# Kernel optimization log

Hardware: AMD Instinct MI355X
Metric: run time of the kernel (lower is better)

The kernel has to match this reference:

```python
import jax, jax.numpy as jnp
import numpy as np

B, T, D = 4096, 200, 128
K_SHORT = 5


def setup_inputs() -> dict:
    key = jax.random.key(0)
    ks = jax.random.split(key, 8)
    hist_items = jax.random.normal(ks[0], (B, T, D), dtype=jnp.float32)
    hist_mask = jax.random.randint(ks[1], (B, T), 0, 2).astype(bool)
    hist_mask = hist_mask.at[:, 0].set(True)  # avoid fully-masked rows
    hist_age_hours = jax.random.uniform(ks[2], (B, T), dtype=jnp.float32) * 168.0
    hist_popularity = jax.random.uniform(ks[3], (B, T), dtype=jnp.float32)
    s = 1.0 / float(np.sqrt(D))
    Wq = jax.random.normal(ks[4], (D, D), dtype=jnp.float32) * s
    Wk = jax.random.normal(ks[5], (D, D), dtype=jnp.float32) * s
    Wv = jax.random.normal(ks[6], (D, D), dtype=jnp.float32) * s
    gate_w = jax.random.normal(ks[7], (1, 2), dtype=jnp.float32) * 0.5
    gate_b = jnp.zeros((1,), dtype=jnp.float32)
    ln_gamma = jnp.ones((D,), dtype=jnp.float32)
    ln_beta = jnp.zeros((D,), dtype=jnp.float32)
    decay_alpha = jnp.asarray(0.05, dtype=jnp.float32)
    return {"hist_items": hist_items, "hist_mask": hist_mask,
            "hist_age_hours": hist_age_hours, "hist_popularity": hist_popularity,
            "Wq": Wq, "Wk": Wk, "Wv": Wv, "gate_w": gate_w, "gate_b": gate_b,
            "ln_gamma": ln_gamma, "ln_beta": ln_beta, "decay_alpha": decay_alpha}


def reference(hist_items, hist_mask, hist_age_hours, hist_popularity,
              Wq, Wk, Wv, gate_w, gate_b, ln_gamma, ln_beta, decay_alpha):
    dt = hist_items.dtype
    maskf = hist_mask.astype(dt)  # (B,T)
    # learnable time-decay bias
    alpha = jax.nn.softplus(decay_alpha) + 1e-6
    decay = jnp.exp(-alpha * hist_age_hours) * maskf  # (B,T)
    # masked mean of history as the single query
    mean_hist = (hist_items * maskf[..., None]).sum(1) / (maskf.sum(1, keepdims=True) + 1e-6)  # (B,D)
    q = mean_hist @ Wq.T                                # (B,D)
    k = jnp.einsum('btd,ed->bte', hist_items, Wk)       # (B,T,D)
    v = jnp.einsum('btd,ed->bte', hist_items, Wv)       # (B,T,D)
    scale = 1.0 / float(np.sqrt(hist_items.shape[-1]))
    scores = jnp.einsum('bd,btd->bt', q, k) * scale + jnp.log(decay + 1e-12)
    scores = jnp.where(hist_mask, scores, -jnp.inf)
    attn = jax.nn.softmax(scores, axis=-1)              # (B,T)
    long_term = jnp.einsum('bt,btd->bd', attn, v)       # (B,D)
    # vectorized last-K window: positions [cnt-K, cnt)
    cnt = jnp.maximum(hist_mask.sum(1), 1)              # (B,) int
    K = min(K_SHORT, hist_items.shape[1])
    ar = jnp.arange(hist_items.shape[1])[None, :]       # (1,T)
    lastk = (ar >= (cnt[:, None] - K)) & (ar < cnt[:, None])  # (B,T) bool
    lk = lastk.astype(dt)
    denom = jnp.maximum(lk.sum(1, keepdims=True), 1.0)  # (B,1)
    short_term = (hist_items * lk[..., None]).sum(1) / denom  # (B,D)
    mean_pop = (hist_popularity * lk).sum(1) / denom[:, 0]
    mean_rec = (hist_age_hours * lk).sum(1) / denom[:, 0]
    ctx = jnp.stack([mean_pop, mean_rec], axis=-1)      # (B,2)
    g = jax.nn.sigmoid(ctx @ gate_w.T + gate_b)         # (B,1)
    user = g * short_term + (1.0 - g) * long_term       # (B,D)
    # LayerNorm (eps=1e-5, biased variance, matching torch)
    mu = user.mean(-1, keepdims=True)
    var = user.var(-1, keepdims=True)
    return (user - mu) / jnp.sqrt(var + 1e-5) * ln_gamma + ln_beta
```

## Files before the change

kernel.cpp:

```cpp
#include <hip/hip_runtime.h>

#define BB 4096
#define TT 200
#define DD 128
#define KSHORT 5
#define RTRIPS 13

__global__ void precompute_A_kernel(const float* __restrict__ Wq,
                                    const float* __restrict__ Wk,
                                    float* __restrict__ A,
                                    const unsigned* __restrict__ m,
                                    int* __restrict__ flag) {
  __shared__ int s_bad;
  const int d = blockIdx.x, dp = threadIdx.x;
  float acc = 0.f;
#pragma unroll 8
  for (int e = 0; e < DD; ++e) acc += Wk[e * DD + d] * Wq[e * DD + dp];
  A[d * DD + dp] = acc * 0.08838834764831845f;
  if (blockIdx.x == 0) {
    if (dp == 0) s_bad = 0;
    __syncthreads();
    unsigned bad = 0;
#pragma unroll
    for (int i = dp; i < 1024; i += DD) bad |= (m[i] > 1u) ? 1u : 0u;
    if (bad) atomicOr(&s_bad, 1);
    __syncthreads();
    if (dp == 0) *flag = s_bad;
  }
}

__global__ __launch_bounds__(256, 4) void fused_kernel(
    const float* __restrict__ items, const void* __restrict__ maskp,
    const float* __restrict__ age, const float* __restrict__ pop,
    const float* __restrict__ Wv, const float* __restrict__ gate_w,
    const float* __restrict__ gate_b, const float* __restrict__ gamma,
    const float* __restrict__ beta, const float* __restrict__ alpha_in,
    const float* __restrict__ A, const int* __restrict__ flagp,
    float* __restrict__ out) {
  __shared__ int   s_idx[TT];
  __shared__ float s_wm[TT], s_ww[TT], s_df[TT];
  __shared__ float s_pa[8 * DD];
  __shared__ float s_pb[8 * DD];
  __shared__ float s_mean[DD], s_qk[DD], s_w[DD], s_user[DD];
  __shared__ float s_l[8];
  __shared__ float s_scal[6];
  __shared__ int   s_wt[4];

  const int b = blockIdx.x, tid = threadIdx.x;
  const int lane32 = tid & 31, stream = tid >> 5;
  const int mode = *flagp;

  float mymask = 0.f, myage = 0.f;
  if (tid < TT) {
    int mk = mode ? (int)((const unsigned char*)maskp)[(size_t)b * TT + tid]
                  : ((const int*)maskp)[(size_t)b * TT + tid];
    mymask = mk ? 1.f : 0.f;
    myage = age[(size_t)b * TT + tid];
    s_wm[tid] = mymask;
  } else if (tid == TT) {
    s_scal[2] = log1pf(expf(alpha_in[0])) + 1e-6f;
  }
  __syncthreads();

  if (tid < 64) {
    float c = 0.f;
    for (int t = tid; t < TT; t += 64) c += s_wm[t];
#pragma unroll
    for (int o = 32; o > 0; o >>= 1) c += __shfl_xor(c, o);
    if (tid == 0) s_scal[0] = c;
  }
  __syncthreads();

  const float cntf = s_scal[0];
  const int cnt = max((int)(cntf + 0.5f), 1);
  const int lo = max(cnt - KSHORT, 0);
  const float dn = (float)(cnt - lo);

  const bool inw = (tid < TT) && (tid >= lo) && (tid < cnt);
  const bool need = (tid < TT) && (mymask > 0.f || inw);
  const unsigned long long bal = __ballot(need);
  const int lane64 = tid & 63, wv = tid >> 6;
  const int within = __popcll(bal & ((1ULL << lane64) - 1ULL));
  if (lane64 == 0) s_wt[wv] = __popcll(bal);
  __syncthreads();

  int off = 0;
#pragma unroll
  for (int w2 = 0; w2 < 3; ++w2) off += (w2 < wv) ? s_wt[w2] : 0;
  const int n = s_wt[0] + s_wt[1] + s_wt[2] + s_wt[3];
  if (need) {
    const int p = off + within;
    const float al = s_scal[2];
    s_idx[p] = tid;
    s_wm[p] = mymask;
    s_ww[p] = inw ? 1.f : 0.f;
    s_df[p] = (mymask > 0.f) ? (__expf(-al * myage) + 1e-12f) : 0.f;
  }
  __syncthreads();

  const float* rowbase = items + (size_t)b * (TT * DD) + lane32 * 4;
  float4 r[RTRIPS];
  float4 ms = {0.f, 0.f, 0.f, 0.f}, ss = {0.f, 0.f, 0.f, 0.f};
#pragma unroll
  for (int j = 0; j < RTRIPS; ++j) {
    const int i = stream + j * 8;
    float4 v = {0.f, 0.f, 0.f, 0.f};
    float wm = 0.f, ww = 0.f;
    if (i < n) {
      const int t = s_idx[i];
      wm = s_wm[i];
      ww = s_ww[i];
      v = *(const float4*)(rowbase + t * DD);
    }
    r[j] = v;
    ms.x += wm * v.x; ms.y += wm * v.y; ms.z += wm * v.z; ms.w += wm * v.w;
    ss.x += ww * v.x; ss.y += ww * v.y; ss.z += ww * v.z; ss.w += ww * v.w;
  }
  for (int i = stream + RTRIPS * 8; i < n; i += 8) {
    const int t = s_idx[i];
    const float wm = s_wm[i], ww = s_ww[i];
    const float4 v = *(const float4*)(rowbase + t * DD);
    ms.x += wm * v.x; ms.y += wm * v.y; ms.z += wm * v.z; ms.w += wm * v.w;
    ss.x += ww * v.x; ss.y += ww * v.y; ss.z += ww * v.z; ss.w += ww * v.w;
  }
  *(float4*)&s_pa[stream * DD + lane32 * 4] = ms;
  *(float4*)&s_pb[stream * DD + lane32 * 4] = ss;
  __syncthreads();

  float short_v = 0.f;
  if (tid < DD) {
    float am = 0.f, as = 0.f;
#pragma unroll
    for (int s = 0; s < 8; ++s) { am += s_pa[s * DD + tid]; as += s_pb[s * DD + tid]; }
    s_mean[tid] = am / (cntf + 1e-6f);
    short_v = as / dn;
  } else if (tid == DD) {
    float sp = 0.f, sr = 0.f;
    for (int t = lo; t < cnt; ++t) {
      sp += pop[(size_t)b * TT + t];
      sr += age[(size_t)b * TT + t];
    }
    const float z = gate_w[0] * (sp / dn) + gate_w[1] * (sr / dn) + gate_b[0];
    s_scal[1] = 1.f / (1.f + expf(-z));
  }
  __syncthreads();

  if (tid < DD) {
    const float4* Ar = (const float4*)(A + tid * DD);
    float acc = 0.f;
#pragma unroll
    for (int j = 0; j < DD / 4; ++j) {
      const float4 a4 = Ar[j];
      acc += a4.x * s_mean[4 * j] + a4.y * s_mean[4 * j + 1] +
             a4.z * s_mean[4 * j + 2] + a4.w * s_mean[4 * j + 3];
    }
    s_qk[tid] = acc;
  }
  __syncthreads();

  const float4 qk = *(const float4*)&s_qk[lane32 * 4];
  float l = 0.f;
  float4 o = {0.f, 0.f, 0.f, 0.f};
#pragma unroll
  for (int j = 0; j < RTRIPS; ++j) {
    const int i = stream + j * 8;
    if (i < n) {
      const float df = s_df[i];
      const float4 v = r[j];
      float p = qk.x * v.x + qk.y * v.y + qk.z * v.z + qk.w * v.w;
      p += __shfl_xor(p, 1);
      p += __shfl_xor(p, 2);
      p += __shfl_xor(p, 4);
      p += __shfl_xor(p, 8);
      p += __shfl_xor(p, 16);
      const float e = __expf(p) * df;
      l += e;
      o.x += e * v.x; o.y += e * v.y; o.z += e * v.z; o.w += e * v.w;
    }
  }
  for (int i = stream + RTRIPS * 8; i < n; i += 8) {
    const int t = s_idx[i];
    const float df = s_df[i];
    const float4 v = *(const float4*)(rowbase + t * DD);
    float p = qk.x * v.x + qk.y * v.y + qk.z * v.z + qk.w * v.w;
    p += __shfl_xor(p, 1);
    p += __shfl_xor(p, 2);
    p += __shfl_xor(p, 4);
    p += __shfl_xor(p, 8);
    p += __shfl_xor(p, 16);
    const float e = __expf(p) * df;
    l += e;
    o.x += e * v.x; o.y += e * v.y; o.z += e * v.z; o.w += e * v.w;
  }
  *(float4*)&s_pa[stream * DD + lane32 * 4] = o;
  if (lane32 == 0) s_l[stream] = l;
  __syncthreads();

  if (tid < DD) {
    float O = 0.f;
#pragma unroll
    for (int s = 0; s < 8; ++s) O += s_pa[s * DD + tid];
    float L = 0.f;
#pragma unroll
    for (int s = 0; s < 8; ++s) L += s_l[s];
    s_w[tid] = O / L;
  }
  __syncthreads();

  if (tid < DD) {
    const float4* Wr = (const float4*)(Wv + tid * DD);
    float acc = 0.f;
#pragma unroll
    for (int j = 0; j < DD / 4; ++j) {
      const float4 a4 = Wr[j];
      acc += a4.x * s_w[4 * j] + a4.y * s_w[4 * j + 1] +
             a4.z * s_w[4 * j + 2] + a4.w * s_w[4 * j + 3];
    }
    const float g = s_scal[1];
    s_user[tid] = g * short_v + (1.f - g) * acc;
  }
  __syncthreads();

  if (tid < 64) {
    const float x0 = s_user[tid], x1 = s_user[64 + tid];
    float su = x0 + x1;
#pragma unroll
    for (int off2 = 32; off2 > 0; off2 >>= 1) su += __shfl_xor(su, off2);
    const float mu = su * (1.f / 128.f);
    const float d0 = x0 - mu, d1 = x1 - mu;
    float s2 = d0 * d0 + d1 * d1;
#pragma unroll
    for (int off2 = 32; off2 > 0; off2 >>= 1) s2 += __shfl_xor(s2, off2);
    if (tid == 0) {
      s_scal[4] = mu;
      s_scal[5] = 1.f / sqrtf(s2 * (1.f / 128.f) + 1e-5f);
    }
  }
  __syncthreads();

  if (tid < DD) {
    out[(size_t)b * DD + tid] =
        (s_user[tid] - s_scal[4]) * s_scal[5] * gamma[tid] + beta[tid];
  }
}

extern "C" void kernel_launch(void* const* d_in, const int* in_sizes, int n_in,
                              void* d_out, int out_size, void* d_ws, size_t ws_size,
                              hipStream_t stream) {
  const float* items  = (const float*)d_in[0];
  const void*  maskp  = d_in[1];
  const float* age    = (const float*)d_in[2];
  const float* pop    = (const float*)d_in[3];
  const float* Wq     = (const float*)d_in[4];
  const float* Wk     = (const float*)d_in[5];
  const float* Wv     = (const float*)d_in[6];
  const float* gate_w = (const float*)d_in[7];
  const float* gate_b = (const float*)d_in[8];
  const float* gamma  = (const float*)d_in[9];
  const float* beta   = (const float*)d_in[10];
  const float* alpha  = (const float*)d_in[11];

  char* ws = (char*)d_ws;
  int*   flag = (int*)ws;
  float* A    = (float*)(ws + 256);
  float* outp = (float*)d_out;

  precompute_A_kernel<<<DD, DD, 0, stream>>>(Wq, Wk, A, (const unsigned*)maskp, flag);
  fused_kernel<<<BB, 256, 0, stream>>>(items, maskp, age, pop, Wv, gate_w,
                                       gate_b, gamma, beta, alpha, A, flag,
                                       outp);
}
```

Before: 589.1 us.

## Fold precompute kernel into fused kernel with per-block q and Wk^T q

Removes the separate precompute launch that formed A = Wk^T Wq and the mask-format flag. Each block now checks the mask format itself, computes q = Wq·mean and then u = Wk^T q in two matvec stages, and counts the mask with a ballot popcount instead of a shared-memory reduction. It also caches the window's popularity and age values in shared memory for the gate. The aim is to save a kernel launch and the dependency between the two kernels. The cost is two matvecs per block instead of one, plus extra barriers, across 4096 blocks.

Result: slower. 603.9 us (+2.5%).

```diff
diff --git a/kernel.cpp b/kernel.cpp
--- a/kernel.cpp
+++ b/kernel.cpp
@@ -6,49 +6,39 @@
 #define KSHORT 5
 #define RTRIPS 13
 
-__global__ void precompute_A_kernel(const float* __restrict__ Wq,
-                                    const float* __restrict__ Wk,
-                                    float* __restrict__ A,
-                                    const unsigned* __restrict__ m,
-                                    int* __restrict__ flag) {
-  __shared__ int s_bad;
-  const int d = blockIdx.x, dp = threadIdx.x;
-  float acc = 0.f;
-#pragma unroll 8
-  for (int e = 0; e < DD; ++e) acc += Wk[e * DD + d] * Wq[e * DD + dp];
-  A[d * DD + dp] = acc * 0.08838834764831845f;
-  if (blockIdx.x == 0) {
-    if (dp == 0) s_bad = 0;
-    __syncthreads();
-    unsigned bad = 0;
-#pragma unroll
-    for (int i = dp; i < 1024; i += DD) bad |= (m[i] > 1u) ? 1u : 0u;
-    if (bad) atomicOr(&s_bad, 1);
-    __syncthreads();
-    if (dp == 0) *flag = s_bad;
-  }
-}
-
 __global__ __launch_bounds__(256, 4) void fused_kernel(
     const float* __restrict__ items, const void* __restrict__ maskp,
     const float* __restrict__ age, const float* __restrict__ pop,
+    const float* __restrict__ Wq, const float* __restrict__ Wk,
     const float* __restrict__ Wv, const float* __restrict__ gate_w,
     const float* __restrict__ gate_b, const float* __restrict__ gamma,
     const float* __restrict__ beta, const float* __restrict__ alpha_in,
-    const float* __restrict__ A, const int* __restrict__ flagp,
     float* __restrict__ out) {
   __shared__ int   s_idx[TT];
-  __shared__ float s_wm[TT], s_ww[TT], s_df[TT];
+  __shared__ float s_cwm[TT], s_cww[TT], s_cdf[TT];
   __shared__ float s_pa[8 * DD];
   __shared__ float s_pb[8 * DD];
-  __shared__ float s_mean[DD], s_qk[DD], s_w[DD], s_user[DD];
+  __shared__ float s_mean[DD], s_q[DD], s_u[DD], s_w[DD], s_user[DD];
+  __shared__ float s_pop[KSHORT], s_agw[KSHORT];
   __shared__ float s_l[8];
   __shared__ float s_scal[6];
-  __shared__ int   s_wt[4];
+  __shared__ int   s_cm[4], s_wt[4];
+  __shared__ int   s_mode;
 
   const int b = blockIdx.x, tid = threadIdx.x;
   const int lane32 = tid & 31, stream = tid >> 5;
-  const int mode = *flagp;
+  const int lane64 = tid & 63, wv = tid >> 6;
+
+  if (tid < 64) {
+    const unsigned* mw = (const unsigned*)maskp;
+    unsigned bad = 0;
+#pragma unroll
+    for (int i = 0; i < 16; ++i) bad |= (mw[tid + 64 * i] > 1u) ? 1u : 0u;
+    const unsigned long long bl = __ballot(bad != 0u);
+    if (tid == 0) s_mode = (bl != 0ULL) ? 1 : 0;
+  }
+  __syncthreads();
+  const int mode = s_mode;
 
   float mymask = 0.f, myage = 0.f;
   if (tid < TT) {
@@ -56,32 +46,28 @@
                   : ((const int*)maskp)[(size_t)b * TT + tid];
     mymask = mk ? 1.f : 0.f;
     myage = age[(size_t)b * TT + tid];
-    s_wm[tid] = mymask;
   } else if (tid == TT) {
     s_scal[2] = log1pf(expf(alpha_in[0])) + 1e-6f;
   }
-  __syncthreads();
-
-  if (tid < 64) {
-    float c = 0.f;
-    for (int t = tid; t < TT; t += 64) c += s_wm[t];
-#pragma unroll
-    for (int o = 32; o > 0; o >>= 1) c += __shfl_xor(c, o);
-    if (tid == 0) s_scal[0] = c;
-  }
-  __syncthreads();
-
-  const float cntf = s_scal[0];
-  const int cnt = max((int)(cntf + 0.5f), 1);
+  const unsigned long long balm = __ballot(mymask > 0.f);
+  if (lane64 == 0) s_cm[wv] = __popcll(balm);
+  __syncthreads();
+
+  const int cm = s_cm[0] + s_cm[1] + s_cm[2] + s_cm[3];
+  const float cntf = (float)cm;
+  const int cnt = max(cm, 1);
   const int lo = max(cnt - KSHORT, 0);
   const float dn = (float)(cnt - lo);
 
-  const bool inw = (tid < TT) && (tid >= lo) && (tid < cnt);
+  const bool inw = (tid >= lo) && (tid < cnt);
   const bool need = (tid < TT) && (mymask > 0.f || inw);
-  const unsigned long long bal = __ballot(need);
-  const int lane64 = tid & 63, wv = tid >> 6;
-  const int within = __popcll(bal & ((1ULL << lane64) - 1ULL));
-  if (lane64 == 0) s_wt[wv] = __popcll(bal);
+  const unsigned long long baln = __ballot(need);
+  const int within = __popcll(baln & ((1ULL << lane64) - 1ULL));
+  if (lane64 == 0) s_wt[wv] = __popcll(baln);
+  if (inw) {
+    s_pop[tid - lo] = pop[(size_t)b * TT + tid];
+    s_agw[tid - lo] = myage;
+  }
   __syncthreads();
 
   int off = 0;
@@ -92,9 +78,9 @@
     const int p = off + within;
     const float al = s_scal[2];
     s_idx[p] = tid;
-    s_wm[p] = mymask;
-    s_ww[p] = inw ? 1.f : 0.f;
-    s_df[p] = (mymask > 0.f) ? (__expf(-al * myage) + 1e-12f) : 0.f;
+    s_cwm[p] = mymask;
+    s_cww[p] = inw ? 1.f : 0.f;
+    s_cdf[p] = (mymask > 0.f) ? (__expf(-al * myage) + 1e-12f) : 0.f;
   }
   __syncthreads();
 
@@ -108,8 +94,8 @@
     float wm = 0.f, ww = 0.f;
     if (i < n) {
       const int t = s_idx[i];
-      wm = s_wm[i];
-      ww = s_ww[i];
+      wm = s_cwm[i];
+      ww = s_cww[i];
       v = *(const float4*)(rowbase + t * DD);
     }
     r[j] = v;
@@ -118,7 +104,7 @@
   }
   for (int i = stream + RTRIPS * 8; i < n; i += 8) {
     const int t = s_idx[i];
-    const float wm = s_wm[i], ww = s_ww[i];
+    const float wm = s_cwm[i], ww = s_cww[i];
     const float4 v = *(const float4*)(rowbase + t * DD);
     ms.x += wm * v.x; ms.y += wm * v.y; ms.z += wm * v.z; ms.w += wm * v.w;
     ss.x += ww * v.x; ss.y += ww * v.y; ss.z += ww * v.z; ss.w += ww * v.w;
@@ -134,38 +120,55 @@
     for (int s = 0; s < 8; ++s) { am += s_pa[s * DD + tid]; as += s_pb[s * DD + tid]; }
     s_mean[tid] = am / (cntf + 1e-6f);
     short_v = as / dn;
+  }
+  __syncthreads();
+
+  if (tid < DD) {
+    const float4* Qr = (const float4*)(Wq + tid * DD);
+    float acc = 0.f;
+#pragma unroll
+    for (int j = 0; j < DD / 4; ++j) {
+      const float4 a4 = Qr[j];
+      acc += a4.x * s_mean[4 * j] + a4.y * s_mean[4 * j + 1] +
+             a4.z * s_mean[4 * j + 2] + a4.w * s_mean[4 * j + 3];
+    }
+    s_q[tid] = acc;
+  }
+  __syncthreads();
+
+  {
+    float4 ua = {0.f, 0.f, 0.f, 0.f};
+    for (int d = stream; d < DD; d += 8) {
+      const float qd = s_q[d];
+      const float4 w4 = *(const float4*)(Wk + d * DD + lane32 * 4);
+      ua.x += qd * w4.x; ua.y += qd * w4.y; ua.z += qd * w4.z; ua.w += qd * w4.w;
+    }
+    *(float4*)&s_pa[stream * DD + lane32 * 4] = ua;
+  }
+  __syncthreads();
+
+  if (tid < DD) {
+    float U = 0.f;
+#pragma unroll
+    for (int s = 0; s < 8; ++s) U += s_pa[s * DD + tid];
+    s_u[tid] = U * 0.08838834764831845f;
   } else if (tid == DD) {
     float sp = 0.f, sr = 0.f;
-    for (int t = lo; t < cnt; ++t) {
-      sp += pop[(size_t)b * TT + t];
-      sr += age[(size_t)b * TT + t];
-    }
+    const int wn = cnt - lo;
+    for (int i = 0; i < wn; ++i) { sp += s_pop[i]; sr += s_agw[i]; }
     const float z = gate_w[0] * (sp / dn) + gate_w[1] * (sr / dn) + gate_b[0];
     s_scal[1] = 1.f / (1.f + expf(-z));
   }
   __syncthreads();
 
-  if (tid < DD) {
-    const float4* Ar = (const float4*)(A + tid * DD);
-    float acc = 0.f;
-#pragma unroll
-    for (int j = 0; j < DD / 4; ++j) {
-      const float4 a4 = Ar[j];
-      acc += a4.x * s_mean[4 * j] + a4.y * s_mean[4 * j + 1] +
-             a4.z * s_mean[4 * j + 2] + a4.w * s_mean[4 * j + 3];
-    }
-    s_qk[tid] = acc;
-  }
-  __syncthreads();
-
-  const float4 qk = *(const float4*)&s_qk[lane32 * 4];
+  const float4 qk = *(const float4*)&s_u[lane32 * 4];
   float l = 0.f;
   float4 o = {0.f, 0.f, 0.f, 0.f};
 #pragma unroll
   for (int j = 0; j < RTRIPS; ++j) {
     const int i = stream + j * 8;
     if (i < n) {
-      const float df = s_df[i];
+      const float df = s_cdf[i];
       const float4 v = r[j];
       float p = qk.x * v.x + qk.y * v.y + qk.z * v.z + qk.w * v.w;
       p += __shfl_xor(p, 1);
@@ -180,7 +183,7 @@
   }
   for (int i = stream + RTRIPS * 8; i < n; i += 8) {
     const int t = s_idx[i];
-    const float df = s_df[i];
+    const float df = s_cdf[i];
     const float4 v = *(const float4*)(rowbase + t * DD);
     float p = qk.x * v.x + qk.y * v.y + qk.z * v.z + qk.w * v.w;
     p += __shfl_xor(p, 1);
@@ -260,13 +263,8 @@
   const float* beta   = (const float*)d_in[10];
   const float* alpha  = (const float*)d_in[11];
 
-  char* ws = (char*)d_ws;
-  int*   flag = (int*)ws;
-  float* A    = (float*)(ws + 256);
   float* outp = (float*)d_out;
-
-  precompute_A_kernel<<<DD, DD, 0, stream>>>(Wq, Wk, A, (const unsigned*)maskp, flag);
-  fused_kernel<<<BB, 256, 0, stream>>>(items, maskp, age, pop, Wv, gate_w,
-                                       gate_b, gamma, beta, alpha, A, flag,
+  fused_kernel<<<BB, 256, 0, stream>>>(items, maskp, age, pop, Wq, Wk, Wv,
+                                       gate_w, gate_b, gamma, beta, alpha,
                                        outp);
 }
```
